# Kernel optimization log

Measured on AMD Instinct MI355X. Metric: run time of the kernel, lower is better.

Reference implementation:

```python
import jax, jax.numpy as jnp
import numpy as np

N_HYP = 128           # HPARAM.HV_NUM_OF_HYPOTHESES
ZSCORE_THR = 2.0      # HPARAM.PRUN_ZSCORE_THRESHOLD
IN_MASK_MULT = 10.0   # HPARAM.HV_HYPOTHESIS_IN_MASK_MULTIPLIER


def setup_inputs() -> dict:
    key = jax.random.key(0)
    k1, k2 = jax.random.split(key)
    B, H, W = 16, 96, 96
    uv_img = jax.random.normal(k1, (B, 2, H, W), dtype=jnp.float32)
    mask = jnp.ones((B, H, W), dtype=bool)  # all-ones mask: pts == full pixel grid
    # stands in for torch.multinomial pair sampling over mask pixels
    pair_idx = jax.random.randint(k2, (B, N_HYP, 2), 0, H * W)
    return {"uv_img": uv_img, "mask": mask, "pair_idx": pair_idx}


def _hough_voting(uv_img, pair_idx):
    B, _, H, W = uv_img.shape
    Np = H * W
    # pts in torch.where(mask) row-major order for an all-ones mask
    ys, xs = jnp.meshgrid(jnp.arange(H), jnp.arange(W), indexing='ij')
    pts = jnp.stack([ys.ravel(), xs.ravel()], axis=1).astype(uv_img.dtype)  # [Np,2]
    uvT = uv_img.reshape(B, 2, Np).transpose(0, 2, 1)                       # [B,Np,2]

    # --- hypothesis generation (pair gather + batched 2x2 pinverse solve) ---
    pp = pts[pair_idx]                                   # [B,N,2(pair),2(yx)]
    p0, p1 = pp[:, :, 0], pp[:, :, 1]                    # [B,N,2]
    uv0 = jnp.take_along_axis(uvT, pair_idx[:, :, 0][:, :, None], axis=1)  # [B,N,2]
    uv1 = jnp.take_along_axis(uvT, pair_idx[:, :, 1][:, :, None], axis=1)  # [B,N,2]
    A = jnp.stack([uv0, -uv1], axis=-1)                  # [B,N,2,2]
    Bvec = (p1 - p0)[..., None]                          # [B,N,2,1]
    X = jnp.linalg.pinv(A) @ Bvec                        # [B,N,2,1]
    s = X[:, :, 0, :]                                    # [B,N,1] scale along ray 0
    Y = s * uv0 + p0                                     # [B,N,2] intersection points

    # --- z-score outlier pruning with mean replacement ---
    mean = jnp.mean(Y, axis=1)                           # [B,2]
    std = jnp.std(Y, axis=1, ddof=1)                     # torch.std is unbiased
    z = (Y - mean[:, None, :]) / std[:, None, :]
    outl = (z > ZSCORE_THR)
    outl = (outl[..., 0] | outl[..., 1])[..., None]
    Yp = jnp.where(outl, mean[:, None, :], Y)

    # --- pairwise vote weighting over all mask pixels ---
    a = Yp[:, :, None, :] - pts[None, None]              # [B,N,Np,2]
    a = a / jnp.linalg.norm(a, axis=-1, keepdims=True)
    votes = jnp.einsum('bnpk,bpk->bnp', a, uvT) > 0      # direction agreement
    w = jnp.sum(votes, axis=-1).astype(uv_img.dtype)     # [B,N]
    match = jnp.trunc(Yp)[:, :, None, :] == pts[None, None]
    h_in_mask = jnp.sum(match[..., 0] & match[..., 1], axis=-1)
    w = jnp.where(h_in_mask == 1, IN_MASK_MULT, 1.0) * w
    w = w / jnp.sum(w, axis=1, keepdims=True)

    # --- NaN guard + weighted mean, swap (y,x)->(x,y) ---
    is_nan = jnp.isnan(Yp[..., 0]) | jnp.isnan(Yp[..., 1])
    Yp = jnp.nan_to_num(Yp)
    w = jnp.where(is_nan, 0.0, w)
    weighted_mean = jnp.sum(Yp * w[..., None], axis=1)   # [B,2]
    return weighted_mean[:, ::-1]


def reference(uv_img, mask, pair_idx):
    # mask is all-ones by construction; pts are the full pixel grid (see _hough_voting)
    return _hough_voting(uv_img, pair_idx)
```

## Files before the change

kernel.cpp:

```cpp
#include <hip/hip_runtime.h>
#include <math.h>

namespace {

constexpr int BATCH = 16;
constexpr int Ww = 96;
constexpr int NP = 96 * 96;
constexpr int NHYP = 128;
constexpr int HPB = 4;
constexpr int GPB = NHYP / HPB;
constexpr int THREADS = 512;

__device__ inline void waveSum2D(double& a, double& b) {
#pragma unroll
  for (int o = 32; o >= 1; o >>= 1) {
    a += __shfl_xor(a, o, 64);
    b += __shfl_xor(b, o, 64);
  }
}
__device__ inline void waveSum2I(int& a, int& b) {
#pragma unroll
  for (int o = 32; o >= 1; o >>= 1) {
    a += __shfl_xor(a, o, 64);
    b += __shfl_xor(b, o, 64);
  }
}
__device__ inline double waveSumD(double v) {
#pragma unroll
  for (int o = 32; o >= 1; o >>= 1) v += __shfl_xor(v, o, 64);
  return v;
}

__global__ __launch_bounds__(THREADS, 4)
void vote_kernel(const float* __restrict__ uv, const int* __restrict__ pair,
                 double* __restrict__ partials ) {
  __shared__ double sPy[NHYP], sPx[NHYP];
  __shared__ float sWm[NHYP];
  __shared__ int sNan[NHYP];
  __shared__ double sh1[2][2], sh2[2][2];
  __shared__ int sC[8][HPB];

  const int t = threadIdx.x;
  const int lane = t & 63;
  const int wv = t >> 6;
  const int b = blockIdx.x >> 5;
  const int g = blockIdx.x & (GPB - 1);
  const float* uvb = uv + (size_t)b * 2 * NP;

  double Yy = 0.0, Yx = 0.0;
  if (t < NHYP) {
    int i0 = pair[(b * NHYP + t) * 2 + 0];
    int i1 = pair[(b * NHYP + t) * 2 + 1];
    double u0 = uvb[i0], v0 = uvb[NP + i0];
    double u1 = uvb[i1], v1 = uvb[NP + i1];
    double y0 = (double)(i0 / Ww), x0 = (double)(i0 % Ww);
    double y1 = (double)(i1 / Ww), x1 = (double)(i1 % Ww);
    double det = u1 * v0 - u0 * v1;
    double s = (u1 * (x1 - x0) - v1 * (y1 - y0)) / det;
    Yy = s * u0 + y0;
    Yx = s * v0 + x0;
  }
  double sy = Yy, sx = Yx;
  waveSum2D(sy, sx);
  if (lane == 0 && wv < 2) { sh1[wv][0] = sy; sh1[wv][1] = sx; }
  __syncthreads();
  const double my = (sh1[0][0] + sh1[1][0]) * (1.0 / NHYP);
  const double mx = (sh1[0][1] + sh1[1][1]) * (1.0 / NHYP);
  const double dy = Yy - my, dx = Yx - mx;
  double qy = dy * dy, qx = dx * dx;
  waveSum2D(qy, qx);
  if (lane == 0 && wv < 2) { sh2[wv][0] = qy; sh2[wv][1] = qx; }
  __syncthreads();
  if (t < NHYP) {
    double vy = (sh2[0][0] + sh2[1][0]) * (1.0 / (NHYP - 1));
    double vx = (sh2[0][1] + sh2[1][1]) * (1.0 / (NHYP - 1));
    bool outl = (dy > 2.0 * sqrt(vy)) || (dx > 2.0 * sqrt(vx));
    double py = outl ? my : Yy;
    double px = outl ? mx : Yx;
    sPy[t] = py;
    sPx[t] = px;
    sWm[t] = (py > -1.0 && py < 96.0 && px > -1.0 && px < 96.0) ? 10.0f : 1.0f;
    sNan[t] = (isnan(py) || isnan(px)) ? 1 : 0;
  }
  __syncthreads();

  const int hb = g * HPB;
  float yy[HPB], yx[HPB];
#pragma unroll
  for (int h = 0; h < HPB; ++h) {
    yy[h] = (float)sPy[hb + h];
    yx[h] = (float)sPx[hb + h];
  }
  int c[HPB] = {0, 0, 0, 0};
#pragma unroll
  for (int it = 0; it < 4; ++it) {
    const int p = (it * THREADS + t) * 4;
    const float4 u4 = *(const float4*)(uvb + p);
    const float4 v4 = *(const float4*)(uvb + NP + p);
    const int yi = p / Ww;
    const float fy = (float)yi;
    const float fx = (float)(p - yi * Ww);
    const float k0 = fy * u4.x + fx * v4.x;
    const float k1 = fy * u4.y + (fx + 1.0f) * v4.y;
    const float k2 = fy * u4.z + (fx + 2.0f) * v4.z;
    const float k3 = fy * u4.w + (fx + 3.0f) * v4.w;
#pragma unroll
    for (int h = 0; h < HPB; ++h) {
      c[h] += (fmaf(yy[h], u4.x, yx[h] * v4.x) > k0) ? 1 : 0;
      c[h] += (fmaf(yy[h], u4.y, yx[h] * v4.y) > k1) ? 1 : 0;
      c[h] += (fmaf(yy[h], u4.z, yx[h] * v4.z) > k2) ? 1 : 0;
      c[h] += (fmaf(yy[h], u4.w, yx[h] * v4.w) > k3) ? 1 : 0;
    }
  }
  {
    const int p = 4 * THREADS * 4 + t * 2;
    const float2 u2 = *(const float2*)(uvb + p);
    const float2 v2 = *(const float2*)(uvb + NP + p);
    const int yi = p / Ww;
    const float fy = (float)yi;
    const float fx = (float)(p - yi * Ww);
    const float k0 = fy * u2.x + fx * v2.x;
    const float k1 = fy * u2.y + (fx + 1.0f) * v2.y;
#pragma unroll
    for (int h = 0; h < HPB; ++h) {
      c[h] += (fmaf(yy[h], u2.x, yx[h] * v2.x) > k0) ? 1 : 0;
      c[h] += (fmaf(yy[h], u2.y, yx[h] * v2.y) > k1) ? 1 : 0;
    }
  }
  waveSum2I(c[0], c[1]);
  waveSum2I(c[2], c[3]);
  if (lane == 0) {
#pragma unroll
    for (int h = 0; h < HPB; ++h) sC[wv][h] = c[h];
  }
  __syncthreads();

  if (t == 0) {
    double wsum = 0.0, ny = 0.0, nx = 0.0;
#pragma unroll
    for (int h = 0; h < HPB; ++h) {
      const int hh = hb + h;
      int cnt = 0;
#pragma unroll
      for (int w8 = 0; w8 < 8; ++w8) cnt += sC[w8][h];
      if (!sNan[hh]) {
        double w = (double)cnt * (double)sWm[hh];
        wsum += w;
        ny += sPy[hh] * w;
        nx += sPx[hh] * w;
      }
    }
    double* slot = partials + (size_t)b * 3 * GPB;
    slot[0 * GPB + g] = wsum;
    slot[1 * GPB + g] = ny;
    slot[2 * GPB + g] = nx;
  }
}

__global__ __launch_bounds__(192)
void final_kernel(const double* __restrict__ partials,
                  float* __restrict__ out) {
  __shared__ double sD[3];
  const int t = threadIdx.x;
  const int lane = t & 63;
  const int wv = t >> 6;
  const int b = blockIdx.x;

  double val = (lane < GPB)
                   ? partials[((size_t)b * 3 + wv) * GPB + lane]
                   : 0.0;
  val = waveSumD(val);
  if (lane == 0) sD[wv] = val;
  __syncthreads();
  if (t == 0) {
    double wsum = sD[0];
    out[b * 2 + 0] = (float)(sD[2] / wsum);
    out[b * 2 + 1] = (float)(sD[1] / wsum);
  }
}

}

extern "C" void kernel_launch(void* const* d_in, const int* in_sizes, int n_in,
                              void* d_out, int out_size, void* d_ws, size_t ws_size,
                              hipStream_t stream) {
  const float* uv = (const float*)d_in[0];
  const int* pair = (const int*)d_in[2];
  float* out = (float*)d_out;

  double* partials = (double*)d_ws;

  vote_kernel<<<BATCH * GPB, THREADS, 0, stream>>>(uv, pair, partials);
  final_kernel<<<BATCH, 192, 0, stream>>>(partials, out);
}
```

Measured before the change: 14.38 us.

## Double hypotheses per block and use 1024-thread blocks for voting

Each block now evaluates 8 hypotheses instead of 4 over the full pixel grid with 1024 threads, halving the block count to 256. The idea is to amortise the per-block hypothesis generation, z-score reductions and pixel loads over more hypotheses. The final per-block combine is spread across 8 threads with a shuffle reduction instead of a serial loop on one thread. Costs: 1024-thread blocks with launch_bounds min 4 put heavy pressure on registers, and with fewer blocks each CU sees less parallelism.

```diff
diff --git a/kernel.cpp b/kernel.cpp
--- a/kernel.cpp
+++ b/kernel.cpp
@@ -7,9 +7,9 @@
 constexpr int Ww = 96;
 constexpr int NP = 96 * 96;
 constexpr int NHYP = 128;
-constexpr int HPB = 4;
+constexpr int HPB = 8;
 constexpr int GPB = NHYP / HPB;
-constexpr int THREADS = 512;
+constexpr int THREADS = 1024;
 
 __device__ inline void waveSum2D(double& a, double& b) {
 #pragma unroll
@@ -38,12 +38,12 @@
   __shared__ float sWm[NHYP];
   __shared__ int sNan[NHYP];
   __shared__ double sh1[2][2], sh2[2][2];
-  __shared__ int sC[8][HPB];
+  __shared__ int sC[16][HPB];
 
   const int t = threadIdx.x;
   const int lane = t & 63;
   const int wv = t >> 6;
-  const int b = blockIdx.x >> 5;
+  const int b = blockIdx.x >> 4;
   const int g = blockIdx.x & (GPB - 1);
   const float* uvb = uv + (size_t)b * 2 * NP;
 
@@ -91,9 +91,9 @@
     yy[h] = (float)sPy[hb + h];
     yx[h] = (float)sPx[hb + h];
   }
-  int c[HPB] = {0, 0, 0, 0};
+  int c[HPB] = {0, 0, 0, 0, 0, 0, 0, 0};
 #pragma unroll
-  for (int it = 0; it < 4; ++it) {
+  for (int it = 0; it < 2; ++it) {
     const int p = (it * THREADS + t) * 4;
     const float4 u4 = *(const float4*)(uvb + p);
     const float4 v4 = *(const float4*)(uvb + NP + p);
@@ -113,47 +113,50 @@
     }
   }
   {
-    const int p = 4 * THREADS * 4 + t * 2;
-    const float2 u2 = *(const float2*)(uvb + p);
-    const float2 v2 = *(const float2*)(uvb + NP + p);
+    const int p = 2 * THREADS * 4 + t;
+    const float u = uvb[p];
+    const float v = uvb[NP + p];
     const int yi = p / Ww;
     const float fy = (float)yi;
     const float fx = (float)(p - yi * Ww);
-    const float k0 = fy * u2.x + fx * v2.x;
-    const float k1 = fy * u2.y + (fx + 1.0f) * v2.y;
+    const float k = fy * u + fx * v;
 #pragma unroll
-    for (int h = 0; h < HPB; ++h) {
-      c[h] += (fmaf(yy[h], u2.x, yx[h] * v2.x) > k0) ? 1 : 0;
-      c[h] += (fmaf(yy[h], u2.y, yx[h] * v2.y) > k1) ? 1 : 0;
-    }
+    for (int h = 0; h < HPB; ++h)
+      c[h] += (fmaf(yy[h], u, yx[h] * v) > k) ? 1 : 0;
   }
   waveSum2I(c[0], c[1]);
   waveSum2I(c[2], c[3]);
+  waveSum2I(c[4], c[5]);
+  waveSum2I(c[6], c[7]);
   if (lane == 0) {
 #pragma unroll
     for (int h = 0; h < HPB; ++h) sC[wv][h] = c[h];
   }
   __syncthreads();
 
-  if (t == 0) {
-    double wsum = 0.0, ny = 0.0, nx = 0.0;
+  if (t < HPB) {
+    int cnt = 0;
 #pragma unroll
-    for (int h = 0; h < HPB; ++h) {
-      const int hh = hb + h;
-      int cnt = 0;
+    for (int w16 = 0; w16 < 16; ++w16) cnt += sC[w16][t];
+    const int hh = hb + t;
+    double w = 0.0, ny = 0.0, nx = 0.0;
+    if (!sNan[hh]) {
+      w = (double)cnt * (double)sWm[hh];
+      ny = sPy[hh] * w;
+      nx = sPx[hh] * w;
+    }
 #pragma unroll
-      for (int w8 = 0; w8 < 8; ++w8) cnt += sC[w8][h];
-      if (!sNan[hh]) {
-        double w = (double)cnt * (double)sWm[hh];
-        wsum += w;
-        ny += sPy[hh] * w;
-        nx += sPx[hh] * w;
-      }
+    for (int o = 4; o >= 1; o >>= 1) {
+      w  += __shfl_xor(w, o, 64);
+      ny += __shfl_xor(ny, o, 64);
+      nx += __shfl_xor(nx, o, 64);
     }
-    double* slot = partials + (size_t)b * 3 * GPB;
-    slot[0 * GPB + g] = wsum;
-    slot[1 * GPB + g] = ny;
-    slot[2 * GPB + g] = nx;
+    if (t == 0) {
+      double* slot = partials + (size_t)b * 3 * GPB;
+      slot[0 * GPB + g] = w;
+      slot[1 * GPB + g] = ny;
+      slot[2 * GPB + g] = nx;
+    }
   }
 }
 
```

Measured after the change: 14.73 us. 2.4% more time.
